# Performance work log

Measured on AMD Instinct MI355X. Metric: run time of the kernel, lower is better.

The kernel has to match this reference:

```python
import jax, jax.numpy as jnp
import numpy as np

P = 4        # patch_size
H = 16       # num_heads
C = 32       # num_channels
E = C * P ** 3  # embed dim = 2048


def setup_inputs() -> dict:
    key = jax.random.key(0)
    ks = jax.random.split(key, 6)
    s = 0.02
    x = jax.random.normal(ks[0], (4, C, 64, 64, 64), dtype=jnp.float32)
    in_proj_w = jax.random.normal(ks[1], (3 * E, E), dtype=jnp.float32) * s
    in_proj_b = jnp.zeros((3 * E,), dtype=jnp.float32)
    out_proj_w = jax.random.normal(ks[2], (E, E), dtype=jnp.float32) * s
    out_proj_b = jnp.zeros((E,), dtype=jnp.float32)
    mlp_w = jax.random.normal(ks[3], (E, E), dtype=jnp.float32) * s
    mlp_b = jnp.zeros((E,), dtype=jnp.float32)
    return {"x": x, "in_proj_w": in_proj_w, "in_proj_b": in_proj_b,
            "out_proj_w": out_proj_w, "out_proj_b": out_proj_b,
            "mlp_w": mlp_w, "mlp_b": mlp_b}


def reference(x, in_proj_w, in_proj_b, out_proj_w, out_proj_b, mlp_w, mlp_b):
    B, Cc, Rx, Ry, Rz = x.shape
    Nx, Ny, Nz = Rx // P, Ry // P, Rz // P
    N = Nx * Ny * Nz
    hd = E // H

    # --- window partition (torch unfold x3) -> (B, C, Nx, Ny, Nz, px, py, pz)
    xw = x.reshape(B, Cc, Nx, P, Ny, P, Nz, P).transpose(0, 1, 2, 4, 6, 3, 5, 7)
    # -> (B, N, C*p^3); torch then feeds MHA with batch_first=False,
    # so seq_len = B and batch = N (attention mixes across the B axis!)
    tok = xw.reshape(B, Cc, N, P, P, P).transpose(0, 2, 1, 3, 4, 5).reshape(B, N, E)

    # --- multi-head attention (seq = B, batch = N)
    qkv = tok @ in_proj_w.T + in_proj_b            # (B, N, 3E)
    q, k, v = jnp.split(qkv, 3, axis=-1)
    q = q.reshape(B, N, H, hd)
    k = k.reshape(B, N, H, hd)
    v = v.reshape(B, N, H, hd)
    scale = 1.0 / jnp.sqrt(jnp.asarray(hd, dtype=q.dtype))
    scores = jnp.einsum('snhd,tnhd->nhst', q * scale, k)   # (N, H, B, B)
    attn = jax.nn.softmax(scores, axis=-1)
    o = jnp.einsum('nhst,tnhd->snhd', attn, v).reshape(B, N, E)
    o = o @ out_proj_w.T + out_proj_b

    # --- mlp
    o = o @ mlp_w.T + mlp_b

    # --- window reverse, matching the torch.cat-based reassembly:
    # out[b,c, px*Nx+nx, py*Ny+ny, pz*Nz+nz] = x8[b,c,nx,ny,nz,px,py,pz]
    x8 = o.reshape(B, N, Cc, P, P, P).transpose(0, 2, 1, 3, 4, 5)
    x8 = x8.reshape(B, Cc, Nx, Ny, Nz, P, P, P)
    out = x8.transpose(0, 1, 5, 2, 6, 3, 7, 4).reshape(B, Cc, Rx, Ry, Rz)
    return out
```

## Files before the change

### kernel.cpp

```cpp
#include <hip/hip_runtime.h>
#include <stdio.h>


typedef __attribute__((ext_vector_type(4))) float f32x4;
typedef __attribute__((ext_vector_type(8))) short s16x8;
typedef __attribute__((ext_vector_type(2))) unsigned short u16x2;
typedef __attribute__((ext_vector_type(4))) unsigned short u16x4;

#define NB 4
#define NC 32
#define NTOK 4096
#define ED 2048
#define NH 16
#define HD 128

__device__ __forceinline__ unsigned short f2bf(float f) {
    union { float f; unsigned int u; } v; v.f = f;
    unsigned int r = (v.u + 0x7fffu + ((v.u >> 16) & 1u)) >> 16;
    return (unsigned short)r;
}
__device__ __forceinline__ float bf2f(unsigned short u) {
    union { unsigned int u; float f; } v; v.u = ((unsigned int)u) << 16;
    return v.f;
}

#define BARRIER() asm volatile("s_barrier" ::: "memory")
#define LGKM0() do { asm volatile("s_waitcnt lgkmcnt(0)" ::: "memory"); \
                     __builtin_amdgcn_sched_barrier(0); } while (0)
#define VMCNT(n) asm volatile("s_waitcnt vmcnt(" #n ")" ::: "memory")

__global__ void f32_to_bf16_kernel(const float* __restrict__ src,
                                   unsigned short* __restrict__ dst, int n4) {
    int i = blockIdx.x * blockDim.x + threadIdx.x;
    if (i >= n4) return;
    f32x4 v = *(const f32x4*)(src + (size_t)i * 4);
    u16x4 w;
    w.x = f2bf(v.x); w.y = f2bf(v.y); w.z = f2bf(v.z); w.w = f2bf(v.w);
    *(u16x4*)(dst + (size_t)i * 4) = w;
}

__global__ __launch_bounds__(256) void transpose_bf16_kernel(
    const float* __restrict__ src, unsigned short* __restrict__ dst, int n) {
    __shared__ float lds[64][68];
    const int bx = blockIdx.x * 64;
    const int by = blockIdx.y * 64;
    const int t  = threadIdx.x;
    const int r  = t >> 2;
    const int c4 = (t & 3) * 16;
    const float* s = src + (size_t)(by + r) * n + bx + c4;
    #pragma unroll
    for (int i = 0; i < 4; ++i)
        *(f32x4*)&lds[r][c4 + i * 4] = *(const f32x4*)(s + i * 4);
    __syncthreads();
    unsigned short* d = dst + (size_t)(bx + r) * n + by + c4;
    #pragma unroll
    for (int i = 0; i < 4; ++i) {
        u16x4 w;
        w.x = f2bf(lds[c4 + i * 4 + 0][r]);
        w.y = f2bf(lds[c4 + i * 4 + 1][r]);
        w.z = f2bf(lds[c4 + i * 4 + 2][r]);
        w.w = f2bf(lds[c4 + i * 4 + 3][r]);
        *(u16x4*)(d + i * 4) = w;
    }
}

__global__ __launch_bounds__(256) void bcomb_kernel(
    const float* __restrict__ mlp_w, const float* __restrict__ opb,
    const float* __restrict__ mlpb, float* __restrict__ bcomb) {
    const int wave = threadIdx.x >> 6, lane = threadIdx.x & 63;
    const int row = blockIdx.x * 4 + wave;
    const float* r = mlp_w + (size_t)row * ED;
    float s = 0.0f;
    for (int k = lane * 4; k < ED; k += 256) {
        f32x4 a = *(const f32x4*)(r + k);
        f32x4 b = *(const f32x4*)(opb + k);
        s += a.x * b.x + a.y * b.y + a.z * b.z + a.w * b.w;
    }
    #pragma unroll
    for (int off = 32; off > 0; off >>= 1) s += __shfl_xor(s, off, 64);
    if (lane == 0) bcomb[row] = s + mlpb[row];
}

__global__ void partition_kernel(const float* __restrict__ x,
                                 unsigned short* __restrict__ tok) {
    int idx = blockIdx.x * blockDim.x + threadIdx.x;
    int m = idx & 15;
    int t = idx >> 4;
    int Y = t & 63; t >>= 6;
    int X = t & 63; t >>= 6;
    int c = t & 31;
    int b = t >> 5;
    f32x4 xv = *(const f32x4*)(x + (size_t)idx * 4);
    int nx = X >> 2, px = X & 3;
    int ny = Y >> 2, py = Y & 3;
    int n = nx * 256 + ny * 16 + m;
    int e = c * 64 + px * 16 + py * 4;
    size_t dst = (size_t)(b * NTOK + n) * ED + e;
    u16x4 w;
    w.x = f2bf(xv.x); w.y = f2bf(xv.y); w.z = f2bf(xv.z); w.w = f2bf(xv.w);
    *(u16x4*)&tok[dst] = w;
}

__global__ __launch_bounds__(256) void gemm128(
    const unsigned short* __restrict__ A,
    const unsigned short* __restrict__ W,
    const float* __restrict__ bias,
    unsigned short* __restrict__ C,
    int M, int Nout, int K)
{
    __shared__ unsigned short ldsA[128 * 64];
    __shared__ unsigned short ldsW[128 * 64];

    const int tid  = threadIdx.x;
    const int wave = tid >> 6;
    const int lane = tid & 63;
    const int bm = blockIdx.x * 128;
    const int bn = blockIdx.y * 128;
    const int wm = (wave >> 1) * 64;
    const int wn = (wave & 1) * 64;

    f32x4 acc[4][4] = {};

    const int srow = lane >> 3;
    const int scol = (lane & 7) * 8;
    const int lrow = lane & 15;
    const int lk   = (lane >> 4) * 8;

    const int nkt = K >> 6;
    for (int kt = 0; kt < nkt; ++kt) {
        const int kbase = kt * 64;
        #pragma unroll
        for (int q = 0; q < 4; ++q) {
            int chunk = wave * 4 + q;
            int row = chunk * 8 + srow;
            const unsigned short* ga = A + (size_t)(bm + row) * K + kbase + scol;
            const unsigned short* gw = W + (size_t)(bn + row) * K + kbase + scol;
            __builtin_amdgcn_global_load_lds(
                (const __attribute__((address_space(1))) void*)ga,
                (__attribute__((address_space(3))) void*)(&ldsA[chunk * 512]),
                16, 0, 0);
            __builtin_amdgcn_global_load_lds(
                (const __attribute__((address_space(1))) void*)gw,
                (__attribute__((address_space(3))) void*)(&ldsW[chunk * 512]),
                16, 0, 0);
        }
        __syncthreads();

        #pragma unroll
        for (int ks = 0; ks < 2; ++ks) {
            const int k0 = ks * 32 + lk;
            s16x8 af[4], bf[4];
            #pragma unroll
            for (int m = 0; m < 4; ++m)
                af[m] = *(const s16x8*)&ldsA[(wm + m * 16 + lrow) * 64 + k0];
            #pragma unroll
            for (int n = 0; n < 4; ++n)
                bf[n] = *(const s16x8*)&ldsW[(wn + n * 16 + lrow) * 64 + k0];
            #pragma unroll
            for (int m = 0; m < 4; ++m)
                #pragma unroll
                for (int n = 0; n < 4; ++n)
                    acc[m][n] = __builtin_amdgcn_mfma_f32_16x16x32_bf16(
                        af[m], bf[n], acc[m][n], 0, 0, 0);
        }
        __syncthreads();
    }

    const int col   = lane & 15;
    const int rbase = (lane >> 4) * 4;
    #pragma unroll
    for (int n = 0; n < 4; ++n) {
        int cc = bn + wn + n * 16 + col;
        float bv = bias[cc];
        #pragma unroll
        for (int m = 0; m < 4; ++m)
            #pragma unroll
            for (int r = 0; r < 4; ++r) {
                int rr = bm + wm + m * 16 + rbase + r;
                C[(size_t)rr * Nout + cc] = f2bf(acc[m][n][r] + bv);
            }
    }
}

template <int OUT_MODE>
__global__ __launch_bounds__(512, 2) void gemm256(
    const unsigned short* __restrict__ A,
    const unsigned short* __restrict__ W,
    const float* __restrict__ bias,
    void* __restrict__ Cv,
    int M, int Nout, int K)
{
    __shared__ unsigned short ldsA[2][2][128 * 64];
    __shared__ unsigned short ldsB[2][2][128 * 64];

    const int tid  = threadIdx.x;
    const int wave = tid >> 6;
    const int lane = tid & 63;

    const int f   = blockIdx.x;
    const int xcd = f & 7;
    const int r_  = f >> 3;
    const int mac = r_ >> 5;
    const int w_  = r_ & 31;
    const int bm  = (xcd * 8 + (w_ & 7)) * 256;
    const int bn  = (mac * 4 + (w_ >> 3)) * 256;

    const int wi    = wave >> 2;
    const int wj    = wave & 3;
    const int bhalf = wj >> 1;
    const int bcol  = (wj & 1) * 64;

    const int lrow = lane & 15;
    const int kq   = lane >> 4;
    const int s0   = ((kq ^ (lrow & 7)) << 3);

    f32x4 acc[8][4] = {};

    const int nkt = K >> 6;

    const int srl   = lane >> 3;
    const int sslot = (((lane & 7) ^ srl) << 3);

    auto stA = [&](int db, int half, int tt) {
        const unsigned short* gb = A + (size_t)(bm + half * 128) * K + tt * 64;
        unsigned short* lb = &ldsA[db][half][0];
        #pragma unroll
        for (int q = 0; q < 2; ++q) {
            const int r0 = wave * 16 + q * 8;
            const unsigned short* ga = gb + (size_t)(r0 + srl) * K + sslot;
            __builtin_amdgcn_global_load_lds(
                (const __attribute__((address_space(1))) void*)ga,
                (__attribute__((address_space(3))) void*)(lb + r0 * 64),
                16, 0, 0);
        }
    };
    auto stB = [&](int db, int half, int tt) {
        const unsigned short* gb = W + (size_t)(bn + half * 128) * K + tt * 64;
        unsigned short* lb = &ldsB[db][half][0];
        #pragma unroll
        for (int q = 0; q < 2; ++q) {
            const int r0 = wave * 16 + q * 8;
            const unsigned short* ga = gb + (size_t)(r0 + srl) * K + sslot;
            __builtin_amdgcn_global_load_lds(
                (const __attribute__((address_space(1))) void*)ga,
                (__attribute__((address_space(3))) void*)(lb + r0 * 64),
                16, 0, 0);
        }
    };

    stA(0, 0, 0); stA(0, 1, 0);
    stB(0, 0, 0); stB(0, 1, 0);
    stA(1, 0, 1); stA(1, 1, 1);
    VMCNT(4);
    BARRIER();

    for (int t = 0; t < nkt; ++t) {
        const int db = t & 1;
        const unsigned short* hA = &ldsA[db][wi][0];
        const unsigned short* hB = &ldsB[db][bhalf][0];

        s16x8 a[8][2], bl[2][2], bh[2][2];

        #pragma unroll
        for (int m = 0; m < 8; ++m) {
            const int rb = (m * 16 + lrow) * 64;
            a[m][0] = *(const s16x8*)&hA[rb + s0];
            a[m][1] = *(const s16x8*)&hA[rb + (s0 ^ 32)];
        }
        #pragma unroll
        for (int n = 0; n < 2; ++n) {
            const int rb = (bcol + n * 16 + lrow) * 64;
            bl[n][0] = *(const s16x8*)&hB[rb + s0];
            bl[n][1] = *(const s16x8*)&hB[rb + (s0 ^ 32)];
        }
        if (t + 1 < nkt) { stB(db ^ 1, 0, t + 1); stB(db ^ 1, 1, t + 1); }
        LGKM0();
        __builtin_amdgcn_s_setprio(1);
        #pragma unroll
        for (int m = 0; m < 8; ++m)
            #pragma unroll
            for (int n = 0; n < 2; ++n) {
                acc[m][n] = __builtin_amdgcn_mfma_f32_16x16x32_bf16(a[m][0], bl[n][0], acc[m][n], 0, 0, 0);
                acc[m][n] = __builtin_amdgcn_mfma_f32_16x16x32_bf16(a[m][1], bl[n][1], acc[m][n], 0, 0, 0);
            }
        __builtin_amdgcn_s_setprio(0);
        BARRIER();

        #pragma unroll
        for (int n = 0; n < 2; ++n) {
            const int rb = (bcol + (n + 2) * 16 + lrow) * 64;
            bh[n][0] = *(const s16x8*)&hB[rb + s0];
            bh[n][1] = *(const s16x8*)&hB[rb + (s0 ^ 32)];
        }
        if (t + 2 < nkt) { stA(db, 0, t + 2); stA(db, 1, t + 2); }
        LGKM0();
        __builtin_amdgcn_s_setprio(1);
        #pragma unroll
        for (int m = 0; m < 8; ++m)
            #pragma unroll
            for (int n = 0; n < 2; ++n) {
                acc[m][n + 2] = __builtin_amdgcn_mfma_f32_16x16x32_bf16(a[m][0], bh[n][0], acc[m][n + 2], 0, 0, 0);
                acc[m][n + 2] = __builtin_amdgcn_mfma_f32_16x16x32_bf16(a[m][1], bh[n][1], acc[m][n + 2], 0, 0, 0);
            }
        __builtin_amdgcn_s_setprio(0);
        if (t + 2 < nkt)      { VMCNT(4); }
        else                  { VMCNT(0); }
        BARRIER();
    }

    const int rowbase = bm + wi * 128 + (kq << 2);
    const int colbase = bn + wj * 64 + lrow;
    float bv[4];
    #pragma unroll
    for (int n = 0; n < 4; ++n) bv[n] = bias[colbase + n * 16];

    if (OUT_MODE == 1) {
        unsigned short* C = (unsigned short*)Cv;
        #pragma unroll
        for (int m = 0; m < 8; ++m) {
            #pragma unroll
            for (int r = 0; r < 4; ++r) {
                const int rr = rowbase + m * 16 + r;
                #pragma unroll
                for (int n = 0; n < 4; ++n) {
                    const int cc = colbase + n * 16;
                    C[(size_t)rr * Nout + cc] = f2bf(acc[m][n][r] + bv[n]);
                }
            }
        }
    } else {
        float* outp = (float*)Cv;
        #pragma unroll
        for (int n = 0; n < 4; ++n) {
            const int cc = colbase + n * 16;
            const int c  = cc >> 6, px = (cc >> 4) & 3,
                      py = (cc >> 2) & 3, pz = cc & 3;
            #pragma unroll
            for (int m = 0; m < 8; ++m) {
                const int rr0 = rowbase + m * 16;
                const int b   = rr0 >> 12, nx = (rr0 >> 8) & 15,
                          ny  = (rr0 >> 4) & 15, nz0 = rr0 & 15;
                float* dst = outp
                    + ((size_t)((b * NC + c) * 64 + px * 16 + nx)) * 4096
                    + (size_t)(py * 16 + ny) * 64 + pz * 16 + nz0;
                f32x4 w = {acc[m][n][0] + bv[n], acc[m][n][1] + bv[n],
                           acc[m][n][2] + bv[n], acc[m][n][3] + bv[n]};
                *(f32x4*)dst = w;
            }
        }
    }
}

__global__ __launch_bounds__(512) void attn_kernel(
    const unsigned short* __restrict__ qkv, unsigned short* __restrict__ o)
{
    const int n    = blockIdx.x;
    const int wave = threadIdx.x >> 6;
    const int lane = threadIdx.x & 63;
    const int h    = wave * 2 + (lane >> 5);
    const int dl   = (lane & 31) * 4;
    const float scale = 0.0883883476483184405501f;

    float q[4][4], k[4][4], v[4][4];
    #pragma unroll
    for (int b = 0; b < 4; ++b) {
        size_t base = (size_t)(b * NTOK + n) * (3 * ED) + h * HD + dl;
        u16x4 uq = *(const u16x4*)&qkv[base];
        u16x4 uk = *(const u16x4*)&qkv[base + ED];
        u16x4 uv = *(const u16x4*)&qkv[base + 2 * ED];
        #pragma unroll
        for (int i = 0; i < 4; ++i) {
            q[b][i] = bf2f(uq[i]); k[b][i] = bf2f(uk[i]); v[b][i] = bf2f(uv[i]);
        }
    }

    float sc[4][4];
    #pragma unroll
    for (int s = 0; s < 4; ++s) {
        #pragma unroll
        for (int t = 0; t < 4; ++t) {
            float p = q[s][0] * k[t][0] + q[s][1] * k[t][1]
                    + q[s][2] * k[t][2] + q[s][3] * k[t][3];
            #pragma unroll
            for (int off = 16; off > 0; off >>= 1)
                p += __shfl_xor(p, off, 64);
            sc[s][t] = p * scale;
        }
    }

    #pragma unroll
    for (int s = 0; s < 4; ++s) {
        float mx = fmaxf(fmaxf(sc[s][0], sc[s][1]), fmaxf(sc[s][2], sc[s][3]));
        float e0 = __expf(sc[s][0] - mx);
        float e1 = __expf(sc[s][1] - mx);
        float e2 = __expf(sc[s][2] - mx);
        float e3 = __expf(sc[s][3] - mx);
        float inv = 1.0f / (e0 + e1 + e2 + e3);
        u16x4 ov;
        #pragma unroll
        for (int i = 0; i < 4; ++i) {
            float oo = (e0 * v[0][i] + e1 * v[1][i] + e2 * v[2][i] + e3 * v[3][i]) * inv;
            ov[i] = f2bf(oo);
        }
        *(u16x4*)&o[(size_t)(s * NTOK + n) * ED + h * HD + dl] = ov;
    }
}

extern "C" void kernel_launch(void* const* d_in, const int* in_sizes, int n_in,
                              void* d_out, int out_size, void* d_ws, size_t ws_size,
                              hipStream_t stream) {
    const float* x          = (const float*)d_in[0];
    const float* in_proj_w  = (const float*)d_in[1];
    const float* in_proj_b  = (const float*)d_in[2];
    const float* out_proj_w = (const float*)d_in[3];
    const float* out_proj_b = (const float*)d_in[4];
    const float* mlp_w      = (const float*)d_in[5];
    const float* mlp_b      = (const float*)d_in[6];
    float* out = (float*)d_out;

    const size_t M = 16384;
    char* ws = (char*)d_ws;
    size_t off = 0;
    unsigned short* tok    = (unsigned short*)(ws + off); off += M * ED * 2;
    unsigned short* w_in   = (unsigned short*)(ws + off); off += (size_t)3 * ED * ED * 2;
    unsigned short* w_mlp  = (unsigned short*)(ws + off); off += (size_t)ED * ED * 2;
    unsigned short* w_outT = (unsigned short*)(ws + off); off += (size_t)ED * ED * 2;
    unsigned short* w_comb = (unsigned short*)(ws + off); off += (size_t)ED * ED * 2;
    float* zbias           = (float*)(ws + off);          off += ED * 4;
    float* b_comb          = (float*)(ws + off);          off += ED * 4;
    unsigned short* obuf   = (unsigned short*)(ws + off); off += M * ED * 2;
    unsigned short* qkv    = (unsigned short*)(ws + off); off += M * 3 * ED * 2;

    if (ws_size < off) {
        fprintf(stderr, "kernel_launch: ws too small (%zu < %zu)\n", ws_size, off);
        return;
    }

    {
        int n4 = 3 * ED * ED / 4;
        f32_to_bf16_kernel<<<(n4 + 255) / 256, 256, 0, stream>>>(in_proj_w, w_in, n4);
        n4 = ED * ED / 4;
        f32_to_bf16_kernel<<<(n4 + 255) / 256, 256, 0, stream>>>(mlp_w, w_mlp, n4);
        transpose_bf16_kernel<<<dim3(ED / 64, ED / 64), 256, 0, stream>>>(
            out_proj_w, w_outT, ED);
        hipMemsetAsync(zbias, 0, ED * sizeof(float), stream);
    }

    gemm128<<<dim3(ED / 128, ED / 128), 256, 0, stream>>>(
        w_mlp, w_outT, zbias, w_comb, ED, ED, ED);
    bcomb_kernel<<<ED / 4, 256, 0, stream>>>(mlp_w, out_proj_b, mlp_b, b_comb);

    partition_kernel<<<(NB * NC * 64 * 64 * 16) / 256, 256, 0, stream>>>(x, tok);

    gemm256<1><<<dim3(64 * (6144 / 256)), 512, 0, stream>>>(
        tok, w_in, in_proj_b, qkv, 16384, 6144, 2048);

    attn_kernel<<<NTOK, 512, 0, stream>>>(qkv, obuf);

    gemm256<2><<<dim3(64 * (2048 / 256)), 512, 0, stream>>>(
        obuf, w_comb, b_comb, out, 16384, 2048, 2048);
}
```

Baseline: 666.7 us.

## Software-pipeline LDS fragment loads across k-halves in bf16 GEMM main loop

Restructures the GEMM inner loop so the first k-half (s0) fragments of the next tile are loaded from LDS at the end of the previous iteration. The second-half (s1) loads are then issued while MFMAs run on already-resident data, using a partial lgkmcnt wait instead of a full drain. The aim is to hide LDS read latency behind matrix math and drop one barrier phase per iteration. The cost is more live vector registers for the double fragment sets, which may lower occupancy or cause spills.

```diff
diff --git a/kernel.cpp b/kernel.cpp
--- a/kernel.cpp
+++ b/kernel.cpp
@@ -27,7 +27,10 @@
 #define BARRIER() asm volatile("s_barrier" ::: "memory")
 #define LGKM0() do { asm volatile("s_waitcnt lgkmcnt(0)" ::: "memory"); \
                      __builtin_amdgcn_sched_barrier(0); } while (0)
+#define LGKM12() do { asm volatile("s_waitcnt lgkmcnt(12)" ::: "memory"); \
+                      __builtin_amdgcn_sched_barrier(0); } while (0)
 #define VMCNT(n) asm volatile("s_waitcnt vmcnt(" #n ")" ::: "memory")
+#define SEAM() __builtin_amdgcn_sched_barrier(0)
 
 __global__ void f32_to_bf16_kernel(const float* __restrict__ src,
                                    unsigned short* __restrict__ dst, int n4) {
@@ -213,6 +216,7 @@
     const int lrow = lane & 15;
     const int kq   = lane >> 4;
     const int s0   = ((kq ^ (lrow & 7)) << 3);
+    const int s1   = s0 ^ 32;
 
     f32x4 acc[8][4] = {};
 
@@ -248,64 +252,88 @@
         }
     };
 
+    s16x8 A0[8], B0[4], A1[8], B1[4];
+
     stA(0, 0, 0); stA(0, 1, 0);
     stB(0, 0, 0); stB(0, 1, 0);
     stA(1, 0, 1); stA(1, 1, 1);
     VMCNT(4);
     BARRIER();
+    {
+        const unsigned short* hA = &ldsA[0][wi][0];
+        const unsigned short* hB = &ldsB[0][bhalf][0];
+        #pragma unroll
+        for (int m = 0; m < 8; ++m)
+            A0[m] = *(const s16x8*)&hA[(m * 16 + lrow) * 64 + s0];
+        #pragma unroll
+        for (int n = 0; n < 2; ++n) {
+            B0[n]     = *(const s16x8*)&hB[(bcol + n * 16 + lrow) * 64 + s0];
+            B0[n + 2] = *(const s16x8*)&hB[(bcol + (n + 2) * 16 + lrow) * 64 + s0];
+        }
+    }
+    SEAM();
 
     for (int t = 0; t < nkt; ++t) {
         const int db = t & 1;
         const unsigned short* hA = &ldsA[db][wi][0];
         const unsigned short* hB = &ldsB[db][bhalf][0];
 
-        s16x8 a[8][2], bl[2][2], bh[2][2];
-
-        #pragma unroll
-        for (int m = 0; m < 8; ++m) {
-            const int rb = (m * 16 + lrow) * 64;
-            a[m][0] = *(const s16x8*)&hA[rb + s0];
-            a[m][1] = *(const s16x8*)&hA[rb + (s0 ^ 32)];
-        }
+        #pragma unroll
+        for (int m = 0; m < 8; ++m)
+            A1[m] = *(const s16x8*)&hA[(m * 16 + lrow) * 64 + s1];
         #pragma unroll
         for (int n = 0; n < 2; ++n) {
-            const int rb = (bcol + n * 16 + lrow) * 64;
-            bl[n][0] = *(const s16x8*)&hB[rb + s0];
-            bl[n][1] = *(const s16x8*)&hB[rb + (s0 ^ 32)];
-        }
+            B1[n]     = *(const s16x8*)&hB[(bcol + n * 16 + lrow) * 64 + s1];
+            B1[n + 2] = *(const s16x8*)&hB[(bcol + (n + 2) * 16 + lrow) * 64 + s1];
+        }
+        SEAM();
+
         if (t + 1 < nkt) { stB(db ^ 1, 0, t + 1); stB(db ^ 1, 1, t + 1); }
+
+        LGKM12();
+        __builtin_amdgcn_s_setprio(1);
+        #pragma unroll
+        for (int m = 0; m < 8; ++m)
+            #pragma unroll
+            for (int n = 0; n < 2; ++n) {
+                acc[m][n]     = __builtin_amdgcn_mfma_f32_16x16x32_bf16(A0[m], B0[n],     acc[m][n],     0, 0, 0);
+                acc[m][n + 2] = __builtin_amdgcn_mfma_f32_16x16x32_bf16(A0[m], B0[n + 2], acc[m][n + 2], 0, 0, 0);
+            }
+        __builtin_amdgcn_s_setprio(0);
+        SEAM();
+
         LGKM0();
+        BARRIER();
+        if (t + 2 < nkt) { stA(db, 0, t + 2); stA(db, 1, t + 2); }
+
         __builtin_amdgcn_s_setprio(1);
         #pragma unroll
         for (int m = 0; m < 8; ++m)
             #pragma unroll
             for (int n = 0; n < 2; ++n) {
-                acc[m][n] = __builtin_amdgcn_mfma_f32_16x16x32_bf16(a[m][0], bl[n][0], acc[m][n], 0, 0, 0);
-                acc[m][n] = __builtin_amdgcn_mfma_f32_16x16x32_bf16(a[m][1], bl[n][1], acc[m][n], 0, 0, 0);
+                acc[m][n]     = __builtin_amdgcn_mfma_f32_16x16x32_bf16(A1[m], B1[n],     acc[m][n],     0, 0, 0);
+                acc[m][n + 2] = __builtin_amdgcn_mfma_f32_16x16x32_bf16(A1[m], B1[n + 2], acc[m][n + 2], 0, 0, 0);
             }
         __builtin_amdgcn_s_setprio(0);
-        BARRIER();
-
-        #pragma unroll
-        for (int n = 0; n < 2; ++n) {
-            const int rb = (bcol + (n + 2) * 16 + lrow) * 64;
-            bh[n][0] = *(const s16x8*)&hB[rb + s0];
-            bh[n][1] = *(const s16x8*)&hB[rb + (s0 ^ 32)];
-        }
-        if (t + 2 < nkt) { stA(db, 0, t + 2); stA(db, 1, t + 2); }
-        LGKM0();
-        __builtin_amdgcn_s_setprio(1);
-        #pragma unroll
-        for (int m = 0; m < 8; ++m)
-            #pragma unroll
-            for (int n = 0; n < 2; ++n) {
-                acc[m][n + 2] = __builtin_amdgcn_mfma_f32_16x16x32_bf16(a[m][0], bh[n][0], acc[m][n + 2], 0, 0, 0);
-                acc[m][n + 2] = __builtin_amdgcn_mfma_f32_16x16x32_bf16(a[m][1], bh[n][1], acc[m][n + 2], 0, 0, 0);
-            }
-        __builtin_amdgcn_s_setprio(0);
+        SEAM();
+
         if (t + 2 < nkt)      { VMCNT(4); }
         else                  { VMCNT(0); }
         BARRIER();
+
+        if (t + 1 < nkt) {
+            const unsigned short* hA2 = &ldsA[db ^ 1][wi][0];
+            const unsigned short* hB2 = &ldsB[db ^ 1][bhalf][0];
+            #pragma unroll
+            for (int m = 0; m < 8; ++m)
+                A0[m] = *(const s16x8*)&hA2[(m * 16 + lrow) * 64 + s0];
+            #pragma unroll
+            for (int n = 0; n < 2; ++n) {
+                B0[n]     = *(const s16x8*)&hB2[(bcol + n * 16 + lrow) * 64 + s0];
+                B0[n + 2] = *(const s16x8*)&hB2[(bcol + (n + 2) * 16 + lrow) * 64 + s0];
+            }
+        }
+        SEAM();
     }
 
     const int rowbase = bm + wi * 128 + (kq << 2);
```

Measured after the change: 665.3 us. About the same (-0.2%).

## Pre-pack weights into MFMA fragment order and load B directly into registers

Applied to the files above, without the earlier changes.

Adds a pack kernel that converts the weights into a per-strip, per-k-tile layout already in MFMA fragment order. The main GEMM then loads B fragments straight from global memory into registers instead of staging them through LDS. The k-loop is rebuilt so the two k-halves of A are read from LDS separately, with B prefetched one tile ahead in registers. This halves LDS usage and removes the B LDS traffic, at the cost of extra packing passes and more register pressure. B is now read from global memory without LDS sharing, so each wave reads its own 64 columns and waves in the same column reload the same B.

```diff
diff --git a/kernel.cpp b/kernel.cpp
--- a/kernel.cpp
+++ b/kernel.cpp
@@ -26,6 +26,8 @@
 
 #define BARRIER() asm volatile("s_barrier" ::: "memory")
 #define LGKM0() do { asm volatile("s_waitcnt lgkmcnt(0)" ::: "memory"); \
+                     __builtin_amdgcn_sched_barrier(0); } while (0)
+#define LGKM8() do { asm volatile("s_waitcnt lgkmcnt(8)" ::: "memory"); \
                      __builtin_amdgcn_sched_barrier(0); } while (0)
 #define VMCNT(n) asm volatile("s_waitcnt vmcnt(" #n ")" ::: "memory")
 
@@ -62,6 +64,36 @@
         w.w = f2bf(lds[c4 + i * 4 + 3][r]);
         *(u16x4*)(d + i * 4) = w;
     }
+}
+
+template <int SRC_F32>
+__global__ __launch_bounds__(512) void pack_w_kernel(
+    const void* __restrict__ src, unsigned short* __restrict__ dst, int K) {
+    __shared__ unsigned short lds[64][72];
+    const int nkt   = K >> 6;
+    const int strip = blockIdx.x;
+    const int kt    = blockIdx.y;
+    const int t     = threadIdx.x;
+    {
+        const int r = t >> 3, c8 = (t & 7) * 8;
+        if (SRC_F32) {
+            const float* s = (const float*)src + (size_t)(strip * 64 + r) * K + kt * 64 + c8;
+            f32x4 a = *(const f32x4*)s, b = *(const f32x4*)(s + 4);
+            u16x4 w0, w1;
+            w0.x = f2bf(a.x); w0.y = f2bf(a.y); w0.z = f2bf(a.z); w0.w = f2bf(a.w);
+            w1.x = f2bf(b.x); w1.y = f2bf(b.y); w1.z = f2bf(b.z); w1.w = f2bf(b.w);
+            *(u16x4*)&lds[r][c8] = w0; *(u16x4*)&lds[r][c8 + 4] = w1;
+        } else {
+            const unsigned short* s = (const unsigned short*)src + (size_t)(strip * 64 + r) * K + kt * 64 + c8;
+            *(s16x8*)&lds[r][c8] = *(const s16x8*)s;
+        }
+    }
+    __syncthreads();
+    const int fid = t >> 6, lane = t & 63;
+    const int n = fid & 3, kh = fid >> 2, lrow = lane & 15, kq = lane >> 4;
+    s16x8 v = *(const s16x8*)&lds[n * 16 + lrow][kh * 32 + kq * 8];
+    size_t off = (((size_t)strip * nkt + kt) * 8 + fid) * 512 + lane * 8;
+    *(s16x8*)&dst[off] = v;
 }
 
 __global__ __launch_bounds__(256) void bcomb_kernel(
@@ -185,13 +217,12 @@
 template <int OUT_MODE>
 __global__ __launch_bounds__(512, 2) void gemm256(
     const unsigned short* __restrict__ A,
-    const unsigned short* __restrict__ W,
+    const unsigned short* __restrict__ Bp,
     const float* __restrict__ bias,
     void* __restrict__ Cv,
     int M, int Nout, int K)
 {
     __shared__ unsigned short ldsA[2][2][128 * 64];
-    __shared__ unsigned short ldsB[2][2][128 * 64];
 
     const int tid  = threadIdx.x;
     const int wave = tid >> 6;
@@ -205,18 +236,18 @@
     const int bm  = (xcd * 8 + (w_ & 7)) * 256;
     const int bn  = (mac * 4 + (w_ >> 3)) * 256;
 
-    const int wi    = wave >> 2;
-    const int wj    = wave & 3;
-    const int bhalf = wj >> 1;
-    const int bcol  = (wj & 1) * 64;
-
+    const int wi   = wave >> 2;
+    const int wj   = wave & 3;
     const int lrow = lane & 15;
     const int kq   = lane >> 4;
     const int s0   = ((kq ^ (lrow & 7)) << 3);
+    const int s1   = s0 ^ 32;
 
     f32x4 acc[8][4] = {};
 
     const int nkt = K >> 6;
+    const unsigned short* Bbase =
+        Bp + ((size_t)((bn >> 6) + wj) * nkt) * 4096 + lane * 8;
 
     const int srl   = lane >> 3;
     const int sslot = (((lane & 7) ^ srl) << 3);
@@ -234,77 +265,68 @@
                 16, 0, 0);
         }
     };
-    auto stB = [&](int db, int half, int tt) {
-        const unsigned short* gb = W + (size_t)(bn + half * 128) * K + tt * 64;
-        unsigned short* lb = &ldsB[db][half][0];
-        #pragma unroll
-        for (int q = 0; q < 2; ++q) {
-            const int r0 = wave * 16 + q * 8;
-            const unsigned short* ga = gb + (size_t)(r0 + srl) * K + sslot;
-            __builtin_amdgcn_global_load_lds(
-                (const __attribute__((address_space(1))) void*)ga,
-                (__attribute__((address_space(3))) void*)(lb + r0 * 64),
-                16, 0, 0);
-        }
-    };
+
+    s16x8 A0[8], A1[8], Bk0[4], Bk1[4];
 
     stA(0, 0, 0); stA(0, 1, 0);
-    stB(0, 0, 0); stB(0, 1, 0);
     stA(1, 0, 1); stA(1, 1, 1);
-    VMCNT(4);
+    {
+        const unsigned short* fb = Bbase;
+        #pragma unroll
+        for (int j = 0; j < 4; ++j) Bk0[j] = *(const s16x8*)(fb + j * 512);
+        #pragma unroll
+        for (int j = 0; j < 4; ++j) Bk1[j] = *(const s16x8*)(fb + (4 + j) * 512);
+    }
+    VMCNT(0);
     BARRIER();
 
     for (int t = 0; t < nkt; ++t) {
         const int db = t & 1;
         const unsigned short* hA = &ldsA[db][wi][0];
-        const unsigned short* hB = &ldsB[db][bhalf][0];
-
-        s16x8 a[8][2], bl[2][2], bh[2][2];
-
-        #pragma unroll
-        for (int m = 0; m < 8; ++m) {
-            const int rb = (m * 16 + lrow) * 64;
-            a[m][0] = *(const s16x8*)&hA[rb + s0];
-            a[m][1] = *(const s16x8*)&hA[rb + (s0 ^ 32)];
-        }
-        #pragma unroll
-        for (int n = 0; n < 2; ++n) {
-            const int rb = (bcol + n * 16 + lrow) * 64;
-            bl[n][0] = *(const s16x8*)&hB[rb + s0];
-            bl[n][1] = *(const s16x8*)&hB[rb + (s0 ^ 32)];
-        }
-        if (t + 1 < nkt) { stB(db ^ 1, 0, t + 1); stB(db ^ 1, 1, t + 1); }
+        const unsigned short* fbn = Bbase + (size_t)(t + 1) * 4096;
+
+        #pragma unroll
+        for (int m = 0; m < 8; ++m)
+            A0[m] = *(const s16x8*)&hA[(m * 16 + lrow) * 64 + s0];
+        #pragma unroll
+        for (int m = 0; m < 8; ++m)
+            A1[m] = *(const s16x8*)&hA[(m * 16 + lrow) * 64 + s1];
+
+        if (t + 2 < nkt) { VMCNT(8); } else { VMCNT(0); }
+        LGKM8();
+        __builtin_amdgcn_s_setprio(1);
+        #pragma unroll
+        for (int m = 0; m < 8; ++m)
+            #pragma unroll
+            for (int n = 0; n < 4; ++n)
+                acc[m][n] = __builtin_amdgcn_mfma_f32_16x16x32_bf16(
+                    A0[m], Bk0[n], acc[m][n], 0, 0, 0);
+        __builtin_amdgcn_s_setprio(0);
+
+        if (t + 1 < nkt) {
+            #pragma unroll
+            for (int j = 0; j < 4; ++j) Bk0[j] = *(const s16x8*)(fbn + j * 512);
+        }
+
         LGKM0();
+        BARRIER();
+
+        if (t + 2 < nkt) { stA(db, 0, t + 2); stA(db, 1, t + 2); }
+
+        if (t + 2 < nkt) { VMCNT(8); } else { VMCNT(0); }
         __builtin_amdgcn_s_setprio(1);
         #pragma unroll
         for (int m = 0; m < 8; ++m)
             #pragma unroll
-            for (int n = 0; n < 2; ++n) {
-                acc[m][n] = __builtin_amdgcn_mfma_f32_16x16x32_bf16(a[m][0], bl[n][0], acc[m][n], 0, 0, 0);
-                acc[m][n] = __builtin_amdgcn_mfma_f32_16x16x32_bf16(a[m][1], bl[n][1], acc[m][n], 0, 0, 0);
-            }
+            for (int n = 0; n < 4; ++n)
+                acc[m][n] = __builtin_amdgcn_mfma_f32_16x16x32_bf16(
+                    A1[m], Bk1[n], acc[m][n], 0, 0, 0);
         __builtin_amdgcn_s_setprio(0);
-        BARRIER();
-
-        #pragma unroll
-        for (int n = 0; n < 2; ++n) {
-            const int rb = (bcol + (n + 2) * 16 + lrow) * 64;
-            bh[n][0] = *(const s16x8*)&hB[rb + s0];
-            bh[n][1] = *(const s16x8*)&hB[rb + (s0 ^ 32)];
-        }
-        if (t + 2 < nkt) { stA(db, 0, t + 2); stA(db, 1, t + 2); }
-        LGKM0();
-        __builtin_amdgcn_s_setprio(1);
-        #pragma unroll
-        for (int m = 0; m < 8; ++m)
-            #pragma unroll
-            for (int n = 0; n < 2; ++n) {
-                acc[m][n + 2] = __builtin_amdgcn_mfma_f32_16x16x32_bf16(a[m][0], bh[n][0], acc[m][n + 2], 0, 0, 0);
-                acc[m][n + 2] = __builtin_amdgcn_mfma_f32_16x16x32_bf16(a[m][1], bh[n][1], acc[m][n + 2], 0, 0, 0);
-            }
-        __builtin_amdgcn_s_setprio(0);
-        if (t + 2 < nkt)      { VMCNT(4); }
-        else                  { VMCNT(0); }
+
+        if (t + 1 < nkt) {
+            #pragma unroll
+            for (int j = 0; j < 4; ++j) Bk1[j] = *(const s16x8*)(fbn + (4 + j) * 512);
+        }
         BARRIER();
     }
 
@@ -421,25 +443,26 @@
     const size_t M = 16384;
     char* ws = (char*)d_ws;
     size_t off = 0;
-    unsigned short* tok    = (unsigned short*)(ws + off); off += M * ED * 2;
-    unsigned short* w_in   = (unsigned short*)(ws + off); off += (size_t)3 * ED * ED * 2;
-    unsigned short* w_mlp  = (unsigned short*)(ws + off); off += (size_t)ED * ED * 2;
-    unsigned short* w_outT = (unsigned short*)(ws + off); off += (size_t)ED * ED * 2;
-    unsigned short* w_comb = (unsigned short*)(ws + off); off += (size_t)ED * ED * 2;
-    float* zbias           = (float*)(ws + off);          off += ED * 4;
-    float* b_comb          = (float*)(ws + off);          off += ED * 4;
-    unsigned short* obuf   = (unsigned short*)(ws + off); off += M * ED * 2;
-    unsigned short* qkv    = (unsigned short*)(ws + off); off += M * 3 * ED * 2;
+    unsigned short* tok     = (unsigned short*)(ws + off); off += M * ED * 2;
+    unsigned short* w_inP   = (unsigned short*)(ws + off); off += (size_t)3 * ED * ED * 2;
+    unsigned short* w_mlp   = (unsigned short*)(ws + off); off += (size_t)ED * ED * 2;
+    unsigned short* w_outT  = (unsigned short*)(ws + off); off += (size_t)ED * ED * 2;
+    unsigned short* w_comb  = (unsigned short*)(ws + off); off += (size_t)ED * ED * 2;
+    unsigned short* w_combP = (unsigned short*)(ws + off); off += (size_t)ED * ED * 2;
+    float* zbias            = (float*)(ws + off);          off += ED * 4;
+    float* b_comb           = (float*)(ws + off);          off += ED * 4;
+    unsigned short* obuf    = (unsigned short*)(ws + off); off += M * ED * 2;
+    unsigned short* qkv     = (unsigned short*)(ws + off); off += M * 3 * ED * 2;
 
     if (ws_size < off) {
         fprintf(stderr, "kernel_launch: ws too small (%zu < %zu)\n", ws_size, off);
         return;
     }
 
+    pack_w_kernel<1><<<dim3(3 * ED / 64, ED / 64), 512, 0, stream>>>(
+        in_proj_w, w_inP, ED);
     {
-        int n4 = 3 * ED * ED / 4;
-        f32_to_bf16_kernel<<<(n4 + 255) / 256, 256, 0, stream>>>(in_proj_w, w_in, n4);
-        n4 = ED * ED / 4;
+        int n4 = ED * ED / 4;
         f32_to_bf16_kernel<<<(n4 + 255) / 256, 256, 0, stream>>>(mlp_w, w_mlp, n4);
         transpose_bf16_kernel<<<dim3(ED / 64, ED / 64), 256, 0, stream>>>(
             out_proj_w, w_outT, ED);
@@ -448,15 +471,17 @@
 
     gemm128<<<dim3(ED / 128, ED / 128), 256, 0, stream>>>(
         w_mlp, w_outT, zbias, w_comb, ED, ED, ED);
+    pack_w_kernel<0><<<dim3(ED / 64, ED / 64), 512, 0, stream>>>(
+        w_comb, w_combP, ED);
     bcomb_kernel<<<ED / 4, 256, 0, stream>>>(mlp_w, out_proj_b, mlp_b, b_comb);
 
     partition_kernel<<<(NB * NC * 64 * 64 * 16) / 256, 256, 0, stream>>>(x, tok);
 
     gemm256<1><<<dim3(64 * (6144 / 256)), 512, 0, stream>>>(
-        tok, w_in, in_proj_b, qkv, 16384, 6144, 2048);
+        tok, w_inP, in_proj_b, qkv, 16384, 6144, 2048);
 
     attn_kernel<<<NTOK, 512, 0, stream>>>(qkv, obuf);
 
     gemm256<2><<<dim3(64 * (2048 / 256)), 512, 0, stream>>>(
-        obuf, w_comb, b_comb, out, 16384, 2048, 2048);
-}
+        obuf, w_combP, b_comb, out, 16384, 2048, 2048);
+}
```

New measurement: 688.9 us. 1.03x slower.

## Restructure 256x256 GEMM to 16 waves with 64x64 warp tiles

Applied to the files above, without the earlier changes.

The 256x256 GEMM block moves from 8 waves (each owning a 128x64 tile with 8x4 accumulators) to 16 waves of 1024 threads, each owning a 64x64 tile with 4x4 accumulators. The K loop is split into two 32-wide halves with separate LDS fragment loads, and the B-tile split by halves is dropped. This cuts per-wave register pressure and adds more waves for latency hiding. In exchange each wave does less MFMA work per LDS read, so LDS traffic per FLOP rises and barriers are shared across more waves. Launch bounds of (1024,4) may also be hard to satisfy.

```diff
diff --git a/kernel.cpp b/kernel.cpp
--- a/kernel.cpp
+++ b/kernel.cpp
@@ -183,15 +183,15 @@
 }
 
 template <int OUT_MODE>
-__global__ __launch_bounds__(512, 2) void gemm256(
+__global__ __launch_bounds__(1024, 4) void gemm256(
     const unsigned short* __restrict__ A,
     const unsigned short* __restrict__ W,
     const float* __restrict__ bias,
     void* __restrict__ Cv,
     int M, int Nout, int K)
 {
-    __shared__ unsigned short ldsA[2][2][128 * 64];
-    __shared__ unsigned short ldsB[2][2][128 * 64];
+    __shared__ unsigned short ldsA[2][256 * 64];
+    __shared__ unsigned short ldsB[2][256 * 64];
 
     const int tid  = threadIdx.x;
     const int wave = tid >> 6;
@@ -205,28 +205,26 @@
     const int bm  = (xcd * 8 + (w_ & 7)) * 256;
     const int bn  = (mac * 4 + (w_ >> 3)) * 256;
 
-    const int wi    = wave >> 2;
-    const int wj    = wave & 3;
-    const int bhalf = wj >> 1;
-    const int bcol  = (wj & 1) * 64;
-
+    const int wi   = wave >> 2;
+    const int wj   = wave & 3;
     const int lrow = lane & 15;
     const int kq   = lane >> 4;
     const int s0   = ((kq ^ (lrow & 7)) << 3);
-
-    f32x4 acc[8][4] = {};
+    const int s1   = s0 ^ 32;
+
+    f32x4 acc[4][4] = {};
 
     const int nkt = K >> 6;
 
     const int srl   = lane >> 3;
     const int sslot = (((lane & 7) ^ srl) << 3);
 
-    auto stA = [&](int db, int half, int tt) {
-        const unsigned short* gb = A + (size_t)(bm + half * 128) * K + tt * 64;
-        unsigned short* lb = &ldsA[db][half][0];
+    auto stA = [&](int db, int tt) {
+        const unsigned short* gb = A + (size_t)bm * K + tt * 64;
+        unsigned short* lb = &ldsA[db][0];
         #pragma unroll
         for (int q = 0; q < 2; ++q) {
-            const int r0 = wave * 16 + q * 8;
+            const int r0 = (wave * 2 + q) * 8;
             const unsigned short* ga = gb + (size_t)(r0 + srl) * K + sslot;
             __builtin_amdgcn_global_load_lds(
                 (const __attribute__((address_space(1))) void*)ga,
@@ -234,12 +232,12 @@
                 16, 0, 0);
         }
     };
-    auto stB = [&](int db, int half, int tt) {
-        const unsigned short* gb = W + (size_t)(bn + half * 128) * K + tt * 64;
-        unsigned short* lb = &ldsB[db][half][0];
+    auto stB = [&](int db, int tt) {
+        const unsigned short* gb = W + (size_t)bn * K + tt * 64;
+        unsigned short* lb = &ldsB[db][0];
         #pragma unroll
         for (int q = 0; q < 2; ++q) {
-            const int r0 = wave * 16 + q * 8;
+            const int r0 = (wave * 2 + q) * 8;
             const unsigned short* ga = gb + (size_t)(r0 + srl) * K + sslot;
             __builtin_amdgcn_global_load_lds(
                 (const __attribute__((address_space(1))) void*)ga,
@@ -248,68 +246,65 @@
         }
     };
 
-    stA(0, 0, 0); stA(0, 1, 0);
-    stB(0, 0, 0); stB(0, 1, 0);
-    stA(1, 0, 1); stA(1, 1, 1);
-    VMCNT(4);
+    stA(0, 0); stB(0, 0);
+    stA(1, 1);
+    VMCNT(2);
     BARRIER();
+
+    const int arow = wi * 64 + lrow;
+    const int brow = wj * 64 + lrow;
 
     for (int t = 0; t < nkt; ++t) {
         const int db = t & 1;
-        const unsigned short* hA = &ldsA[db][wi][0];
-        const unsigned short* hB = &ldsB[db][bhalf][0];
-
-        s16x8 a[8][2], bl[2][2], bh[2][2];
-
-        #pragma unroll
-        for (int m = 0; m < 8; ++m) {
-            const int rb = (m * 16 + lrow) * 64;
-            a[m][0] = *(const s16x8*)&hA[rb + s0];
-            a[m][1] = *(const s16x8*)&hA[rb + (s0 ^ 32)];
-        }
-        #pragma unroll
-        for (int n = 0; n < 2; ++n) {
-            const int rb = (bcol + n * 16 + lrow) * 64;
-            bl[n][0] = *(const s16x8*)&hB[rb + s0];
-            bl[n][1] = *(const s16x8*)&hB[rb + (s0 ^ 32)];
-        }
-        if (t + 1 < nkt) { stB(db ^ 1, 0, t + 1); stB(db ^ 1, 1, t + 1); }
+        const unsigned short* hA = &ldsA[db][0];
+        const unsigned short* hB = &ldsB[db][0];
+
+        s16x8 af[4], bf[4];
+
+        #pragma unroll
+        for (int m = 0; m < 4; ++m)
+            af[m] = *(const s16x8*)&hA[(arow + m * 16) * 64 + s0];
+        #pragma unroll
+        for (int n = 0; n < 4; ++n)
+            bf[n] = *(const s16x8*)&hB[(brow + n * 16) * 64 + s0];
+        if (t + 1 < nkt) stB(db ^ 1, t + 1);
         LGKM0();
         __builtin_amdgcn_s_setprio(1);
         #pragma unroll
-        for (int m = 0; m < 8; ++m)
-            #pragma unroll
-            for (int n = 0; n < 2; ++n) {
-                acc[m][n] = __builtin_amdgcn_mfma_f32_16x16x32_bf16(a[m][0], bl[n][0], acc[m][n], 0, 0, 0);
-                acc[m][n] = __builtin_amdgcn_mfma_f32_16x16x32_bf16(a[m][1], bl[n][1], acc[m][n], 0, 0, 0);
-            }
+        for (int m = 0; m < 4; ++m)
+            #pragma unroll
+            for (int n = 0; n < 4; ++n)
+                acc[m][n] = __builtin_amdgcn_mfma_f32_16x16x32_bf16(
+                    af[m], bf[n], acc[m][n], 0, 0, 0);
         __builtin_amdgcn_s_setprio(0);
+        __builtin_amdgcn_sched_barrier(0);
+
+        #pragma unroll
+        for (int m = 0; m < 4; ++m)
+            af[m] = *(const s16x8*)&hA[(arow + m * 16) * 64 + s1];
+        #pragma unroll
+        for (int n = 0; n < 4; ++n)
+            bf[n] = *(const s16x8*)&hB[(brow + n * 16) * 64 + s1];
+        LGKM0();
         BARRIER();
-
-        #pragma unroll
-        for (int n = 0; n < 2; ++n) {
-            const int rb = (bcol + (n + 2) * 16 + lrow) * 64;
-            bh[n][0] = *(const s16x8*)&hB[rb + s0];
-            bh[n][1] = *(const s16x8*)&hB[rb + (s0 ^ 32)];
-        }
-        if (t + 2 < nkt) { stA(db, 0, t + 2); stA(db, 1, t + 2); }
-        LGKM0();
+        if (t + 2 < nkt) stA(db, t + 2);
         __builtin_amdgcn_s_setprio(1);
         #pragma unroll
-        for (int m = 0; m < 8; ++m)
-            #pragma unroll
-            for (int n = 0; n < 2; ++n) {
-                acc[m][n + 2] = __builtin_amdgcn_mfma_f32_16x16x32_bf16(a[m][0], bh[n][0], acc[m][n + 2], 0, 0, 0);
-                acc[m][n + 2] = __builtin_amdgcn_mfma_f32_16x16x32_bf16(a[m][1], bh[n][1], acc[m][n + 2], 0, 0, 0);
-            }
+        for (int m = 0; m < 4; ++m)
+            #pragma unroll
+            for (int n = 0; n < 4; ++n)
+                acc[m][n] = __builtin_amdgcn_mfma_f32_16x16x32_bf16(
+                    af[m], bf[n], acc[m][n], 0, 0, 0);
         __builtin_amdgcn_s_setprio(0);
-        if (t + 2 < nkt)      { VMCNT(4); }
+        if (t + 2 < nkt)      { VMCNT(2); }
         else                  { VMCNT(0); }
         BARRIER();
     }
 
-    const int rowbase = bm + wi * 128 + (kq << 2);
-    const int colbase = bn + wj * 64 + lrow;
+    const int col     = lane & 15;
+    const int rbase   = (lane >> 4) * 4;
+    const int rowbase = bm + wi * 64;
+    const int colbase = bn + wj * 64 + col;
     float bv[4];
     #pragma unroll
     for (int n = 0; n < 4; ++n) bv[n] = bias[colbase + n * 16];
@@ -317,15 +312,13 @@
     if (OUT_MODE == 1) {
         unsigned short* C = (unsigned short*)Cv;
         #pragma unroll
-        for (int m = 0; m < 8; ++m) {
+        for (int m = 0; m < 4; ++m) {
             #pragma unroll
             for (int r = 0; r < 4; ++r) {
-                const int rr = rowbase + m * 16 + r;
+                const int rr = rowbase + m * 16 + rbase + r;
                 #pragma unroll
-                for (int n = 0; n < 4; ++n) {
-                    const int cc = colbase + n * 16;
-                    C[(size_t)rr * Nout + cc] = f2bf(acc[m][n][r] + bv[n]);
-                }
+                for (int n = 0; n < 4; ++n)
+                    C[(size_t)rr * Nout + colbase + n * 16] = f2bf(acc[m][n][r] + bv[n]);
             }
         }
     } else {
@@ -336,8 +329,8 @@
             const int c  = cc >> 6, px = (cc >> 4) & 3,
                       py = (cc >> 2) & 3, pz = cc & 3;
             #pragma unroll
-            for (int m = 0; m < 8; ++m) {
-                const int rr0 = rowbase + m * 16;
+            for (int m = 0; m < 4; ++m) {
+                const int rr0 = rowbase + m * 16 + rbase;
                 const int b   = rr0 >> 12, nx = (rr0 >> 8) & 15,
                           ny  = (rr0 >> 4) & 15, nz0 = rr0 & 15;
                 float* dst = outp
@@ -452,11 +445,11 @@
 
     partition_kernel<<<(NB * NC * 64 * 64 * 16) / 256, 256, 0, stream>>>(x, tok);
 
-    gemm256<1><<<dim3(64 * (6144 / 256)), 512, 0, stream>>>(
+    gemm256<1><<<dim3(64 * (6144 / 256)), 1024, 0, stream>>>(
         tok, w_in, in_proj_b, qkv, 16384, 6144, 2048);
 
     attn_kernel<<<NTOK, 512, 0, stream>>>(qkv, obuf);
 
-    gemm256<2><<<dim3(64 * (2048 / 256)), 512, 0, stream>>>(
+    gemm256<2><<<dim3(64 * (2048 / 256)), 1024, 0, stream>>>(
         obuf, w_comb, b_comb, out, 16384, 2048, 2048);
 }
```

Result: slower. 687.5 us (+3.1%).
